# Kernel tuning notes

Hardware: AMD Instinct MI355X
Metric: run time of the kernel (lower is better)

The kernel has to match this reference:

```python
import jax, jax.numpy as jnp
import numpy as np

M = 262144      # total tokens
K = 64          # n_channels (input dim)
N = 64          # expert_size (output dim)
E = 8           # n_experts


def setup_inputs() -> dict:
    key = jax.random.key(0)
    k1, k2, k3 = jax.random.split(key, 3)
    x = jax.random.normal(k1, (M, K), dtype=jnp.float32)
    sel = jax.random.randint(k2, (M,), 0, E, dtype=jnp.int32)
    w = jax.random.normal(k3, (E, K, N), dtype=jnp.float32)
    return {"x": x, "sel": sel, "w": w}


def reference(x, sel, w):
    # cvmm: out[m] = x[m] @ w[sel[m]]  (per-token expert GEMM)
    # Loop over the small fixed expert set; accumulate masked dense GEMMs
    # instead of materializing w[sel] ([M,K,N], which would be huge).
    E_ = w.shape[0]
    out = jnp.zeros((x.shape[0], w.shape[2]), dtype=x.dtype)
    for e in range(E_):
        mask = (sel == e)[:, None]           # [M,1]
        out = out + jnp.where(mask, x @ w[e], jnp.zeros((), x.dtype))
    return out
```

## Files before the change

kernel.cpp:

```cpp
#include <hip/hip_runtime.h>


typedef __bf16 bf16x8 __attribute__((ext_vector_type(8)));
typedef __bf16 bf16x4 __attribute__((ext_vector_type(4)));
typedef float  floatx4 __attribute__((ext_vector_type(4)));

#define NCHUNK 4
#define CHUNK_LDS 8192

__global__ __launch_bounds__(256, 4) void cvmm_kernel(
    const float* __restrict__ x,
    const int* __restrict__ sel,
    const float* __restrict__ w,
    float* __restrict__ out,
    int M)
{
    __shared__ __align__(16) unsigned char lds[2 * CHUNK_LDS];

    const int T    = threadIdx.x;
    const int lane = T & 63;
    const int wv   = T >> 6;
    const int q    = lane >> 4;
    const int l16  = lane & 15;
    const int n0   = wv << 4;

    floatx4 bfp[8][2];
#pragma unroll
    for (int e = 0; e < 8; ++e) {
#pragma unroll
        for (int t = 0; t < 2; ++t) {
            const float* wp = w + ((e * 64 + t * 32 + q * 8) * 64) + (n0 + l16);
            bf16x8 f;
#pragma unroll
            for (int j = 0; j < 8; ++j) f[j] = (__bf16)wp[j * 64];
            bfp[e][t] = __builtin_bit_cast(floatx4, f);
        }
    }
#pragma unroll
    for (int e = 0; e < 8; ++e)
#pragma unroll
        for (int t = 0; t < 2; ++t)
            asm volatile("" : "+v"(bfp[e][t]));

    bf16x8 zf;
#pragma unroll
    for (int j = 0; j < 8; ++j) zf[j] = (__bf16)0.0f;

    const int wrow  = T >> 4;
    const int wbase = wrow * 128 + (((((T & 15) >> 1)) ^ (wrow & 7)) << 4) + (T & 1) * 8;
    const int roff0 = l16 * 128 + (((q    ) ^ (l16 & 7)) << 4);
    const int roff1 = l16 * 128 + (((q + 4) ^ (l16 & 7)) << 4);

    const long tok0 = (long)blockIdx.x * (NCHUNK * 64);

    floatx4 R0, R1, R2, R3;
    int Sc0, Sc1, Sc2, Sc3, Sn0, Sn1, Sn2, Sn3;
    {
        const float* xc = x + tok0 * 64;
        R0 = *(const floatx4*)(xc + 0 * 1024 + 4 * T);
        R1 = *(const floatx4*)(xc + 1 * 1024 + 4 * T);
        R2 = *(const floatx4*)(xc + 2 * 1024 + 4 * T);
        R3 = *(const floatx4*)(xc + 3 * 1024 + 4 * T);
        const int* sp = sel + tok0 + l16;
        Sc0 = sp[0]; Sc1 = sp[16]; Sc2 = sp[32]; Sc3 = sp[48];
    }

    int buf = 0;
#pragma unroll
    for (int c = 0; c < NCHUNK; ++c) {
        unsigned char* lb = &lds[buf * CHUNK_LDS];
#define STAGE(p, Rv)                                                   \
        {                                                              \
            bf16x4 v;                                                  \
            v[0] = (__bf16)Rv[0]; v[1] = (__bf16)Rv[1];                \
            v[2] = (__bf16)Rv[2]; v[3] = (__bf16)Rv[3];                \
            *(bf16x4*)(lb + (p) * 2048 + wbase) = v;                   \
        }
        STAGE(0, R0) STAGE(1, R1) STAGE(2, R2) STAGE(3, R3)
#undef STAGE

        __syncthreads();

        if (c + 1 < NCHUNK) {
            const float* xc = x + (tok0 + (c + 1) * 64) * 64;
            R0 = *(const floatx4*)(xc + 0 * 1024 + 4 * T);
            R1 = *(const floatx4*)(xc + 1 * 1024 + 4 * T);
            R2 = *(const floatx4*)(xc + 2 * 1024 + 4 * T);
            R3 = *(const floatx4*)(xc + 3 * 1024 + 4 * T);
            const int* sp = sel + tok0 + (c + 1) * 64 + l16;
            Sn0 = sp[0]; Sn1 = sp[16]; Sn2 = sp[32]; Sn3 = sp[48];
        }

#pragma unroll
        for (int i = 0; i < 4; ++i) {
            const bf16x8 af0 = *(const bf16x8*)(lb + i * 2048 + roff0);
            const bf16x8 af1 = *(const bf16x8*)(lb + i * 2048 + roff1);
            const int s = (i == 0) ? Sc0 : (i == 1) ? Sc1 : (i == 2) ? Sc2 : Sc3;

            floatx4 c0 = {0.0f, 0.0f, 0.0f, 0.0f};
            floatx4 c1 = {0.0f, 0.0f, 0.0f, 0.0f};
#pragma unroll
            for (int e = 0; e < 8; ++e) {
                const bool ok = (s == e);
                bf16x8 a0m = ok ? af0 : zf;
                bf16x8 a1m = ok ? af1 : zf;
                c0 = __builtin_amdgcn_mfma_f32_16x16x32_bf16(
                         a0m, __builtin_bit_cast(bf16x8, bfp[e][0]), c0, 0, 0, 0);
                c1 = __builtin_amdgcn_mfma_f32_16x16x32_bf16(
                         a1m, __builtin_bit_cast(bf16x8, bfp[e][1]), c1, 0, 0, 0);
            }

            const long m0 = tok0 + c * 64 + i * 16;
            float* op = out + (m0 + q * 4) * 64 + n0 + l16;
#pragma unroll
            for (int r = 0; r < 4; ++r) {
                op[(long)r * 64] = c0[r] + c1[r];
            }
        }

        Sc0 = Sn0; Sc1 = Sn1; Sc2 = Sn2; Sc3 = Sn3;
        buf ^= 1;
    }
}

extern "C" void kernel_launch(void* const* d_in, const int* in_sizes, int n_in,
                              void* d_out, int out_size, void* d_ws, size_t ws_size,
                              hipStream_t stream) {
    const float* x   = (const float*)d_in[0];
    const int*   sel = (const int*)d_in[1];
    const float* w   = (const float*)d_in[2];
    float*       out = (float*)d_out;

    const int M = in_sizes[0] / 64;
    const int blocks = M / (NCHUNK * 64);

    cvmm_kernel<<<blocks, 256, 0, stream>>>(x, sel, w, out, M);
}
```

Measured before the change: 123.5 us.

## Sort tokens by expert per block and prepack bf16 weights in workspace

```diff
diff --git a/kernel.cpp b/kernel.cpp
--- a/kernel.cpp
+++ b/kernel.cpp
@@ -5,17 +5,31 @@
 typedef __bf16 bf16x4 __attribute__((ext_vector_type(4)));
 typedef float  floatx4 __attribute__((ext_vector_type(4)));
 
-#define NCHUNK 4
-#define CHUNK_LDS 8192
+__global__ __launch_bounds__(256) void wpack_kernel(
+    const float* __restrict__ w, bf16x8* __restrict__ wp)
+{
+    const int id   = blockIdx.x * 256 + threadIdx.x;
+    const int lane = id & 63;
+    const int nt   = (id >> 6) & 3;
+    const int t    = (id >> 8) & 1;
+    const int e    = id >> 9;
+    const int q = lane >> 4, l16 = lane & 15;
+    const float* src = w + (((e * 64) + t * 32 + q * 8) * 64) + nt * 16 + l16;
+    bf16x8 f;
+#pragma unroll
+    for (int j = 0; j < 8; ++j) f[j] = (__bf16)src[j * 64];
+    wp[id] = f;
+}
 
-__global__ __launch_bounds__(256, 4) void cvmm_kernel(
+__global__ __launch_bounds__(256, 8) void cvmm_kernel(
     const float* __restrict__ x,
     const int* __restrict__ sel,
-    const float* __restrict__ w,
-    float* __restrict__ out,
-    int M)
+    const bf16x8* __restrict__ wp,
+    float* __restrict__ out)
 {
-    __shared__ __align__(16) unsigned char lds[2 * CHUNK_LDS];
+    __shared__ __align__(16) unsigned char xls[128 * 128];
+    __shared__ unsigned int sortLds[128];
+    __shared__ int wcLds[16];
 
     const int T    = threadIdx.x;
     const int lane = T & 63;
@@ -24,102 +38,85 @@
     const int l16  = lane & 15;
     const int n0   = wv << 4;
 
-    floatx4 bfp[8][2];
+    const long tok0 = (long)blockIdx.x * 128;
+
+    const float* xb = x + tok0 * 64;
+    floatx4 R[8];
 #pragma unroll
-    for (int e = 0; e < 8; ++e) {
+    for (int i = 0; i < 8; ++i)
+        R[i] = *(const floatx4*)(xb + i * 1024 + 4 * T);
+
+    int s = 0, myrank = 0;
+    if (T < 128) {
+        s = sel[tok0 + T];
+        const unsigned long long lt = (1ull << lane) - 1;
 #pragma unroll
-        for (int t = 0; t < 2; ++t) {
-            const float* wp = w + ((e * 64 + t * 32 + q * 8) * 64) + (n0 + l16);
-            bf16x8 f;
-#pragma unroll
-            for (int j = 0; j < 8; ++j) f[j] = (__bf16)wp[j * 64];
-            bfp[e][t] = __builtin_bit_cast(floatx4, f);
+        for (int e = 0; e < 8; ++e) {
+            unsigned long long m = __ballot(s == e);
+            if (s == e) myrank = __popcll(m & lt);
+            if (lane == 0) wcLds[wv * 8 + e] = __popcll(m);
         }
     }
+    __syncthreads();
+    if (T < 128) {
+        int bb = 0;
 #pragma unroll
-    for (int e = 0; e < 8; ++e)
+        for (int e2 = 0; e2 < 8; ++e2) {
+            const int tot = wcLds[e2] + wcLds[8 + e2];
+            if (e2 < s) bb += tot;
+        }
+        const int wb = (wv == 1) ? wcLds[s] : 0;
+        sortLds[bb + wb + myrank] = (unsigned)T | ((unsigned)s << 8);
+    }
+
+    const int wrow = T >> 4;
+    const int g    = (T & 15) >> 1;
+    const int half = (T & 1) * 8;
 #pragma unroll
-        for (int t = 0; t < 2; ++t)
-            asm volatile("" : "+v"(bfp[e][t]));
+    for (int i = 0; i < 8; ++i) {
+        const int row = i * 16 + wrow;
+        bf16x4 v;
+        v[0] = (__bf16)R[i][0]; v[1] = (__bf16)R[i][1];
+        v[2] = (__bf16)R[i][2]; v[3] = (__bf16)R[i][3];
+        *(bf16x4*)(xls + row * 128 + (((g) ^ (row & 7)) << 4) + half) = v;
+    }
+    __syncthreads();
 
     bf16x8 zf;
 #pragma unroll
     for (int j = 0; j < 8; ++j) zf[j] = (__bf16)0.0f;
 
-    const int wrow  = T >> 4;
-    const int wbase = wrow * 128 + (((((T & 15) >> 1)) ^ (wrow & 7)) << 4) + (T & 1) * 8;
-    const int roff0 = l16 * 128 + (((q    ) ^ (l16 & 7)) << 4);
-    const int roff1 = l16 * 128 + (((q + 4) ^ (l16 & 7)) << 4);
-
-    const long tok0 = (long)blockIdx.x * (NCHUNK * 64);
-
-    floatx4 R0, R1, R2, R3;
-    int Sc0, Sc1, Sc2, Sc3, Sn0, Sn1, Sn2, Sn3;
-    {
-        const float* xc = x + tok0 * 64;
-        R0 = *(const floatx4*)(xc + 0 * 1024 + 4 * T);
-        R1 = *(const floatx4*)(xc + 1 * 1024 + 4 * T);
-        R2 = *(const floatx4*)(xc + 2 * 1024 + 4 * T);
-        R3 = *(const floatx4*)(xc + 3 * 1024 + 4 * T);
-        const int* sp = sel + tok0 + l16;
-        Sc0 = sp[0]; Sc1 = sp[16]; Sc2 = sp[32]; Sc3 = sp[48];
-    }
-
-    int buf = 0;
-#pragma unroll
-    for (int c = 0; c < NCHUNK; ++c) {
-        unsigned char* lb = &lds[buf * CHUNK_LDS];
-#define STAGE(p, Rv)                                                   \
-        {                                                              \
-            bf16x4 v;                                                  \
-            v[0] = (__bf16)Rv[0]; v[1] = (__bf16)Rv[1];                \
-            v[2] = (__bf16)Rv[2]; v[3] = (__bf16)Rv[3];                \
-            *(bf16x4*)(lb + (p) * 2048 + wbase) = v;                   \
-        }
-        STAGE(0, R0) STAGE(1, R1) STAGE(2, R2) STAGE(3, R3)
-#undef STAGE
-
-        __syncthreads();
-
-        if (c + 1 < NCHUNK) {
-            const float* xc = x + (tok0 + (c + 1) * 64) * 64;
-            R0 = *(const floatx4*)(xc + 0 * 1024 + 4 * T);
-            R1 = *(const floatx4*)(xc + 1 * 1024 + 4 * T);
-            R2 = *(const floatx4*)(xc + 2 * 1024 + 4 * T);
-            R3 = *(const floatx4*)(xc + 3 * 1024 + 4 * T);
-            const int* sp = sel + tok0 + (c + 1) * 64 + l16;
-            Sn0 = sp[0]; Sn1 = sp[16]; Sn2 = sp[32]; Sn3 = sp[48];
-        }
+    const bf16x8* wpw = wp + wv * 64 + lane;
 
 #pragma unroll
-        for (int i = 0; i < 4; ++i) {
-            const bf16x8 af0 = *(const bf16x8*)(lb + i * 2048 + roff0);
-            const bf16x8 af1 = *(const bf16x8*)(lb + i * 2048 + roff1);
-            const int s = (i == 0) ? Sc0 : (i == 1) ? Sc1 : (i == 2) ? Sc2 : Sc3;
+    for (int i = 0; i < 8; ++i) {
+        const unsigned u = sortLds[i * 16 + l16];
+        const int tokL = (int)(u & 255u);
+        const int el   = (int)(u >> 8);
+        const bf16x8 af0 = *(const bf16x8*)(xls + tokL * 128 + (((q)     ^ (tokL & 7)) << 4));
+        const bf16x8 af1 = *(const bf16x8*)(xls + tokL * 128 + (((q + 4) ^ (tokL & 7)) << 4));
+        const int elo = __builtin_amdgcn_readfirstlane(el);
+        const int ehi = __builtin_amdgcn_readlane(el, 15);
 
-            floatx4 c0 = {0.0f, 0.0f, 0.0f, 0.0f};
-            floatx4 c1 = {0.0f, 0.0f, 0.0f, 0.0f};
-#pragma unroll
-            for (int e = 0; e < 8; ++e) {
-                const bool ok = (s == e);
-                bf16x8 a0m = ok ? af0 : zf;
-                bf16x8 a1m = ok ? af1 : zf;
-                c0 = __builtin_amdgcn_mfma_f32_16x16x32_bf16(
-                         a0m, __builtin_bit_cast(bf16x8, bfp[e][0]), c0, 0, 0, 0);
-                c1 = __builtin_amdgcn_mfma_f32_16x16x32_bf16(
-                         a1m, __builtin_bit_cast(bf16x8, bfp[e][1]), c1, 0, 0, 0);
-            }
-
-            const long m0 = tok0 + c * 64 + i * 16;
-            float* op = out + (m0 + q * 4) * 64 + n0 + l16;
-#pragma unroll
-            for (int r = 0; r < 4; ++r) {
-                op[(long)r * 64] = c0[r] + c1[r];
+        floatx4 acc = {0.0f, 0.0f, 0.0f, 0.0f};
+        if (elo == ehi) {
+            const bf16x8 wf0 = wpw[elo * 512];
+            const bf16x8 wf1 = wpw[elo * 512 + 256];
+            acc = __builtin_amdgcn_mfma_f32_16x16x32_bf16(wf0, af0, acc, 0, 0, 0);
+            acc = __builtin_amdgcn_mfma_f32_16x16x32_bf16(wf1, af1, acc, 0, 0, 0);
+        } else {
+            for (int e = elo; e <= ehi; ++e) {
+                const bf16x8 wf0 = wpw[e * 512];
+                const bf16x8 wf1 = wpw[e * 512 + 256];
+                const bool ok = (el == e);
+                const bf16x8 am0 = ok ? af0 : zf;
+                const bf16x8 am1 = ok ? af1 : zf;
+                acc = __builtin_amdgcn_mfma_f32_16x16x32_bf16(wf0, am0, acc, 0, 0, 0);
+                acc = __builtin_amdgcn_mfma_f32_16x16x32_bf16(wf1, am1, acc, 0, 0, 0);
             }
         }
-
-        Sc0 = Sn0; Sc1 = Sn1; Sc2 = Sn2; Sc3 = Sn3;
-        buf ^= 1;
+        float* op = out + (tok0 + tokL) * 64 + n0 + (q << 2);
+        *(floatx4*)op = acc;
     }
 }
 
@@ -132,7 +129,8 @@
     float*       out = (float*)d_out;
 
     const int M = in_sizes[0] / 64;
-    const int blocks = M / (NCHUNK * 64);
+    bf16x8* wp = (bf16x8*)d_ws;
 
-    cvmm_kernel<<<blocks, 256, 0, stream>>>(x, sel, w, out, M);
+    wpack_kernel<<<16, 256, 0, stream>>>(w, wp);
+    cvmm_kernel<<<M / 128, 256, 0, stream>>>(x, sel, wp, out);
 }
```

Measured after the change: 129.2 us. +4.6%, slower.
